# Performance work log

Measured on AMD Instinct MI355X. Metric: run time of the kernel, lower is better.

## Reference

```python
import jax, jax.numpy as jnp
import numpy as np

NUM_UNIQUE = 256      # unique initial states after unique_bitstrings_with_counts
NUM_SAMPLES = 4096    # expectation_samples (shots per unique circuit)
NUM_QUBITS = 64
BATCH_SIZE = 1024


def setup_inputs() -> dict:
    key = jax.random.key(0)
    k1, k2, k3, k4 = jax.random.split(key, 4)
    # Bitstring samples drawn from each unique transformed circuit (stands in
    # for tfq.layers.Sample output, already densified like .to_tensor()).
    samples = jax.random.randint(k1, (NUM_UNIQUE, NUM_SAMPLES, NUM_QUBITS), 0, 2, dtype=jnp.int32)
    # expand_unique_results gather indices: batch entry -> unique circuit id
    idx = jax.random.randint(k2, (BATCH_SIZE,), 0, NUM_UNIQUE, dtype=jnp.int32)
    # Ising/KOBE energy parameters (observable.energy thetas)
    bias = jax.random.normal(k3, (NUM_QUBITS,), dtype=jnp.float32)
    kernel = jax.random.normal(k4, (NUM_QUBITS, NUM_QUBITS), dtype=jnp.float32) * 0.1
    return {"samples": samples, "idx": idx, "bias": bias, "kernel": kernel}


def reference(samples, idx, bias, kernel):
    # spins s = 1 - 2*b  for bitstrings b in {0,1}
    spins = 1.0 - 2.0 * samples.astype(jnp.float32)          # [c, s, q]
    # observable.energy(x): linear + quadratic Ising energy per bitstring
    lin = jnp.einsum("csq,q->cs", spins, bias)                # [c, s]
    quad = jnp.einsum("csq,qr,csr->cs", spins, kernel, spins)  # [c, s]
    energies = lin + quad
    # tf.map_fn(reduce_mean(energy)) over unique circuits -> [c]
    unique_expectations = jnp.mean(energies, axis=1)
    # expand_unique_results: gather back to full batch, expand_dims(..., 1)
    return unique_expectations[idx][:, None]                  # [batch_size, 1]
```

## Files before the change

kernel.cpp:

```cpp
#include <hip/hip_runtime.h>
#include <stdint.h>

#define NUM_UNIQUE   256
#define NUM_SAMPLES  4096
#define NUM_QUBITS   64
#define BATCH_SIZE   1024
#define THREADS      1024
#define WAVES        (THREADS / 64)
#define CHUNKS       (NUM_SAMPLES / 64)
#define CHUNKS_PER_WAVE (CHUNKS / WAVES)

__global__ __launch_bounds__(THREADS)
void energy_kernel(const int* __restrict__ samples,
                   const float* __restrict__ bias,
                   const float* __restrict__ Kmat,
                   float* __restrict__ uniq)
{
    __shared__ float Klds[NUM_QUBITS * 65];
    __shared__ unsigned long long words[WAVES][64];
    __shared__ float wsum[WAVES];

    const int tid  = threadIdx.x;
    const int wave = tid >> 6;
    const int lane = tid & 63;
    const int c    = blockIdx.x;

    for (int t = tid; t < NUM_QUBITS * NUM_QUBITS; t += THREADS)
        Klds[(t >> 6) * 65 + (t & 63)] = Kmat[t];
    __syncthreads();

    float accQ = 0.0f;
    int   cnt  = 0;

    for (int ci = 0; ci < CHUNKS_PER_WAVE; ++ci) {
        const int chunk = wave * CHUNKS_PER_WAVE + ci;
        const int4* sp = (const int4*)(samples +
            ((size_t)c * NUM_SAMPLES + (size_t)(chunk * 64 + lane)) * NUM_QUBITS);

        unsigned long long w = 0ull;
        #pragma unroll
        for (int i = 0; i < 16; ++i) {
            int4 v = sp[i];
            w |= ((unsigned long long)(v.x & 1)) << (4 * i + 0);
            w |= ((unsigned long long)(v.y & 1)) << (4 * i + 1);
            w |= ((unsigned long long)(v.z & 1)) << (4 * i + 2);
            w |= ((unsigned long long)(v.w & 1)) << (4 * i + 3);
        }

        unsigned long long myB = 0ull;
        #pragma unroll
        for (int q = 0; q < 64; ++q) {
            unsigned long long bq = __ballot((unsigned int)((w >> q) & 1ull));
            myB = (lane == q) ? bq : myB;
        }

        __syncthreads();
        words[wave][lane] = myB;
        __syncthreads();

        cnt += (int)__popcll(myB);

        const float* Krow = &Klds[lane * 65];
        #pragma unroll
        for (int r = 0; r < 64; ++r) {
            unsigned long long br = words[wave][r];
            int pc = (int)__popcll(myB ^ br);
            accQ = fmaf(Krow[r], (float)(64 - 2 * pc), accQ);
        }
    }

    float contrib = accQ +
        bias[lane] * (float)(CHUNKS_PER_WAVE * 64 - 2 * cnt);

    #pragma unroll
    for (int off = 32; off > 0; off >>= 1)
        contrib += __shfl_down(contrib, off);

    if (lane == 0) wsum[wave] = contrib;
    __syncthreads();
    if (tid == 0) {
        float s = 0.0f;
        #pragma unroll
        for (int i = 0; i < WAVES; ++i) s += wsum[i];
        uniq[c] = s * (1.0f / NUM_SAMPLES);
    }
}

__global__ void gather_kernel(const float* __restrict__ uniq,
                              const int* __restrict__ idx,
                              float* __restrict__ out)
{
    int b = blockIdx.x * blockDim.x + threadIdx.x;
    if (b < BATCH_SIZE) out[b] = uniq[idx[b]];
}

extern "C" void kernel_launch(void* const* d_in, const int* in_sizes, int n_in,
                              void* d_out, int out_size, void* d_ws, size_t ws_size,
                              hipStream_t stream)
{
    const int*   samples = (const int*)d_in[0];
    const int*   idx     = (const int*)d_in[1];
    const float* bias    = (const float*)d_in[2];
    const float* Kmat    = (const float*)d_in[3];
    float* out  = (float*)d_out;
    float* uniq = (float*)d_ws;

    energy_kernel<<<NUM_UNIQUE, THREADS, 0, stream>>>(samples, bias, Kmat, uniq);
    gather_kernel<<<(BATCH_SIZE + 255) / 256, 256, 0, stream>>>(uniq, idx, out);
}
```

Before: 377.5 us.

## Coalesce sample loads and transpose bits with shuffles instead of ballots

Each lane now reads int4 elements in a coalesced, lane-strided pattern instead of walking its own 256-byte sample row. The lane's bits are packed into four 16-bit masks, and a four-step shuffle builds each qubit's 64-sample bit word, replacing 64 ballots. The two block-wide barriers per chunk are dropped because the word buffer is wave-private. The term 64-2*popcount is also moved algebraically out of the inner loop using a precomputed K row sum. The risks are a mistake in the bit permutation and reliance on wave-level ordering of the LDS reads and writes with no explicit barrier.

```diff
diff --git a/kernel.cpp b/kernel.cpp
--- a/kernel.cpp
+++ b/kernel.cpp
@@ -29,48 +29,54 @@
         Klds[(t >> 6) * 65 + (t & 63)] = Kmat[t];
     __syncthreads();
 
-    float accQ = 0.0f;
-    int   cnt  = 0;
+    const float* Krow = &Klds[lane * 65];
+    float rowsum = 0.0f;
+    #pragma unroll
+    for (int r = 0; r < 64; ++r) rowsum += Krow[r];
+
+    float pcacc = 0.0f;
+    int   cnt   = 0;
 
     for (int ci = 0; ci < CHUNKS_PER_WAVE; ++ci) {
         const int chunk = wave * CHUNKS_PER_WAVE + ci;
-        const int4* sp = (const int4*)(samples +
-            ((size_t)c * NUM_SAMPLES + (size_t)(chunk * 64 + lane)) * NUM_QUBITS);
+        const int4* cp = (const int4*)(samples +
+            ((size_t)c * NUM_SAMPLES + (size_t)chunk * 64) * NUM_QUBITS);
 
-        unsigned long long w = 0ull;
+        unsigned int m0 = 0, m1 = 0, m2 = 0, m3 = 0;
         #pragma unroll
         for (int i = 0; i < 16; ++i) {
-            int4 v = sp[i];
-            w |= ((unsigned long long)(v.x & 1)) << (4 * i + 0);
-            w |= ((unsigned long long)(v.y & 1)) << (4 * i + 1);
-            w |= ((unsigned long long)(v.z & 1)) << (4 * i + 2);
-            w |= ((unsigned long long)(v.w & 1)) << (4 * i + 3);
+            int4 v = cp[i * 64 + lane];
+            m0 = (m0 << 1) | (unsigned int)(v.x & 1);
+            m1 = (m1 << 1) | (unsigned int)(v.y & 1);
+            m2 = (m2 << 1) | (unsigned int)(v.z & 1);
+            m3 = (m3 << 1) | (unsigned int)(v.w & 1);
+        }
+        unsigned long long W = (unsigned long long)m0
+                             | ((unsigned long long)m1 << 16)
+                             | ((unsigned long long)m2 << 32)
+                             | ((unsigned long long)m3 << 48);
+
+        unsigned long long B = 0ull;
+        #pragma unroll
+        for (int p = 0; p < 4; ++p) {
+            unsigned long long src = __shfl(W, 16 * p + (lane >> 2));
+            B |= ((src >> (16 * (lane & 3))) & 0xFFFFull) << (16 * p);
         }
 
-        unsigned long long myB = 0ull;
-        #pragma unroll
-        for (int q = 0; q < 64; ++q) {
-            unsigned long long bq = __ballot((unsigned int)((w >> q) & 1ull));
-            myB = (lane == q) ? bq : myB;
-        }
+        cnt += (int)__popcll(B);
+        words[wave][lane] = B;
 
-        __syncthreads();
-        words[wave][lane] = myB;
-        __syncthreads();
-
-        cnt += (int)__popcll(myB);
-
-        const float* Krow = &Klds[lane * 65];
+        const unsigned long long* wp = words[wave];
         #pragma unroll
         for (int r = 0; r < 64; ++r) {
-            unsigned long long br = words[wave][r];
-            int pc = (int)__popcll(myB ^ br);
-            accQ = fmaf(Krow[r], (float)(64 - 2 * pc), accQ);
+            unsigned long long br = wp[r];
+            int pc = (int)__popcll(B ^ br);
+            pcacc = fmaf(Krow[r], (float)pc, pcacc);
         }
     }
 
-    float contrib = accQ +
-        bias[lane] * (float)(CHUNKS_PER_WAVE * 64 - 2 * cnt);
+    float contrib = 64.0f * (float)CHUNKS_PER_WAVE * rowsum - 2.0f * pcacc
+                  + bias[lane] * (float)(CHUNKS_PER_WAVE * 64 - 2 * cnt);
 
     #pragma unroll
     for (int off = 32; off > 0; off >>= 1)
```

Result: no change. 371.4 us (-1.6%).
